# Optimization experiments

Hardware: AMD Instinct MI355X
Metric: run time of the kernel (lower is better)

## Reference

```python
import jax, jax.numpy as jnp
import numpy as np
import itertools

DIM = 384
KEY_DIM = 32
NUM_HEADS = 8
ATTN_RATIO = 4
RESOLUTION = 7
D = ATTN_RATIO * KEY_DIM          # 128
DH = D * NUM_HEADS                # 1024
H_QKV = DH + 2 * KEY_DIM * NUM_HEADS  # 1536
B = 2048
N = RESOLUTION ** 2               # 49


def _build_bias_idxs():
    points = list(itertools.product(range(RESOLUTION), range(RESOLUTION)))
    attention_offsets = {}
    idxs = []
    for p1 in points:
        for p2 in points:
            offset = (abs(p1[0] - p2[0]), abs(p1[1] - p2[1]))
            if offset not in attention_offsets:
                attention_offsets[offset] = len(attention_offsets)
            idxs.append(attention_offsets[offset])
    return np.array(idxs, dtype=np.int32).reshape(N, N), len(attention_offsets)


def setup_inputs() -> dict:
    key = jax.random.key(0)
    ks = jax.random.split(key, 6)
    bias_idxs_np, n_offsets = _build_bias_idxs()  # n_offsets == 49 for resolution 7
    x = jax.random.normal(ks[0], (B, N, DIM), dtype=jnp.float32)
    qkv_w = jax.random.normal(ks[1], (H_QKV, DIM), dtype=jnp.float32) * (DIM ** -0.5)
    qkv_b = jnp.zeros((H_QKV,), dtype=jnp.float32)
    proj_w = jax.random.normal(ks[2], (DIM, DH), dtype=jnp.float32) * (DH ** -0.5)
    proj_b = jnp.zeros((DIM,), dtype=jnp.float32)
    attn_bias = jax.random.normal(ks[3], (NUM_HEADS, n_offsets), dtype=jnp.float32) * 0.02
    bias_idxs = jnp.asarray(bias_idxs_np)
    return {"x": x, "qkv_w": qkv_w, "qkv_b": qkv_b, "proj_w": proj_w,
            "proj_b": proj_b, "attn_bias": attn_bias, "bias_idxs": bias_idxs}


def reference(x, qkv_w, qkv_b, proj_w, proj_b, attn_bias, bias_idxs):
    Bb, Nn, _ = x.shape
    scale = KEY_DIM ** -0.5
    qkv = x @ qkv_w.T + qkv_b                       # [B, N, 1536]
    qkv = qkv.reshape(Bb, Nn, NUM_HEADS, KEY_DIM + KEY_DIM + D)
    q = qkv[..., :KEY_DIM]                          # [B, N, H, kd]
    k = qkv[..., KEY_DIM:2 * KEY_DIM]               # [B, N, H, kd]
    v = qkv[..., 2 * KEY_DIM:]                      # [B, N, H, d]
    bias = attn_bias[:, bias_idxs]                  # [H, N, N] gathered rel-pos bias
    attn = jnp.einsum('bnhk,bmhk->bhnm', q, k) * scale + bias
    attn = jax.nn.softmax(attn, axis=-1)
    out = jnp.einsum('bhnm,bmhd->bnhd', attn, v).reshape(Bb, Nn, DH)
    return out @ proj_w.T + proj_b                  # [B, N, dim]
```

## Files before the change

### kernel.cpp

```cpp
#include <hip/hip_runtime.h>
#include <cstddef>
#include <cstdint>

#define TOK    49
#define KD     32
#define NH     8
#define DHEAD  128
#define HQKV   1536
#define DHTOT  1024
#define DIMM   384

typedef unsigned short u16;
typedef float  f32x4  __attribute__((ext_vector_type(4)));
typedef __bf16 bf16x8 __attribute__((ext_vector_type(8)));

typedef const __attribute__((address_space(1))) void gas_void;
typedef __attribute__((address_space(3))) void las_void;

static __device__ __forceinline__ u16 f2bf(float f) {
    unsigned int u = __builtin_bit_cast(unsigned int, f);
    return (u16)((u + 0x7fffu + ((u >> 16) & 1u)) >> 16);
}

static __device__ __forceinline__ int swz(int row, int c) {
    return (row << 6) + ((((c >> 3) ^ (row & 7)) << 3) | (c & 7));
}

static __device__ __forceinline__ int swzV(int row, int c) {
    return (row << 6) + ((((c >> 3) ^ (row & 7) ^ ((row >> 3) & 7)) << 3) | (c & 7));
}

static __device__ __forceinline__ int xcd_chunk(int bid, int nwg) {
    const int xcd = bid & 7, slot = bid >> 3;
    const int q = nwg >> 3, r = nwg & 7;
    return (xcd < r ? xcd * (q + 1) : r * (q + 1) + (xcd - r) * q) + slot;
}

#define BAR() __builtin_amdgcn_s_barrier()
#define WAIT_VM8() asm volatile("s_waitcnt vmcnt(8)" ::: "memory")
#define WAIT_VM0() asm volatile("s_waitcnt vmcnt(0)" ::: "memory")
#define LGKM0_BAR() do { asm volatile("s_waitcnt lgkmcnt(0)" ::: "memory"); \
                         __builtin_amdgcn_s_barrier(); } while (0)

__global__ __launch_bounds__(256)
void cast_swz(const float* __restrict__ in, u16* __restrict__ out, int K8, long nchunk)
{
    long i = (long)blockIdx.x * 256 + threadIdx.x;
    const long stride = (long)gridDim.x * 256;
    for (; i < nchunk; i += stride) {
        const long row = i / K8;
        const int  c8  = (int)(i - row * K8);
        const int  slot = c8 & 7, tpan = c8 >> 3;
        float4 v0 = reinterpret_cast<const float4*>(in)[i * 2];
        float4 v1 = reinterpret_cast<const float4*>(in)[i * 2 + 1];
        uint4 o;
        o.x = f2bf(v0.x) | ((unsigned)f2bf(v0.y) << 16);
        o.y = f2bf(v0.z) | ((unsigned)f2bf(v0.w) << 16);
        o.z = f2bf(v1.x) | ((unsigned)f2bf(v1.y) << 16);
        o.w = f2bf(v1.z) | ((unsigned)f2bf(v1.w) << 16);
        *reinterpret_cast<uint4*>(out + row * (long)K8 * 8 + tpan * 64 +
                                  ((slot ^ ((int)row & 7)) << 3)) = o;
    }
}

__global__ __launch_bounds__(256)
void bias_expand(const float* __restrict__ attn_bias, const int* __restrict__ idxs,
                 float* __restrict__ bias_full, int n_off)
{
    int i = blockIdx.x * 256 + threadIdx.x;
    if (i < NH * TOK * TOK) {
        int h = i / (TOK * TOK), s = i - h * (TOK * TOK);
        bias_full[i] = attn_bias[h * n_off + idxs[s]];
    }
}

static __device__ __forceinline__ int frag_off(int row, int ks8fg) {
    return (row << 6) + (((ks8fg ^ (row & 7)) << 3));
}

__global__ __launch_bounds__(256)
void gemm_qkv(const u16* __restrict__ A,
              const u16* __restrict__ W,
              const float* __restrict__ bias,
              u16* __restrict__ qkvb, int M)
{
    const int K = DIMM;
    const int NB = HQKV / 128;
    const int nwg = (M / 128) * NB;
    const int wgid = xcd_chunk(blockIdx.x, nwg);
    const int bm = (wgid / NB) * 128;
    const int bn = (wgid % NB) * 128;

    __shared__ u16 Alds[2][128 * 64];
    __shared__ u16 Blds[2][128 * 64];

    const int t    = threadIdx.x;
    const int lane = t & 63;
    const int wv   = t >> 6;
    const int wr   = wv >> 1;
    const int wc   = wv & 1;

    const int lrow = lane >> 3;
    const int lcol = (lane & 7) * 8;
    const int frow = lane & 15;
    const int fg   = lane >> 4;

    f32x4 acc[4][4];
    #pragma unroll
    for (int mi = 0; mi < 4; ++mi)
        #pragma unroll
        for (int ni = 0; ni < 4; ++ni) acc[mi][ni] = (f32x4)0.0f;

    auto STAGE = [&](int buf, int k0) {
        #pragma unroll
        for (int i = 0; i < 4; ++i) {
            const int c   = i * 4 + wv;
            const int row = c * 8 + lrow;
            __builtin_amdgcn_global_load_lds((gas_void*)(A + (size_t)(bm + row) * K + k0 + lcol),
                                             (las_void*)(&Alds[buf][c * 512]), 16, 0, 0);
            __builtin_amdgcn_global_load_lds((gas_void*)(W + (size_t)(bn + row) * K + k0 + lcol),
                                             (las_void*)(&Blds[buf][c * 512]), 16, 0, 0);
        }
    };

    STAGE(0, 0);
    STAGE(1, 64);

    const int NT = 6;
    for (int ts = 0; ts < NT; ++ts) {
        if (ts < NT - 1) { WAIT_VM8(); }
        else             { WAIT_VM0(); }
        BAR();
        const u16* Ab = Alds[ts & 1];
        const u16* Bb = Blds[ts & 1];
        #pragma unroll
        for (int ks = 0; ks < 2; ++ks) {
            const int sl = ks * 4 + fg;
            bf16x8 af[4], bf[4];
            #pragma unroll
            for (int mi = 0; mi < 4; ++mi)
                af[mi] = *reinterpret_cast<const bf16x8*>(&Ab[frag_off(wr * 64 + mi * 16 + frow, sl)]);
            #pragma unroll
            for (int ni = 0; ni < 4; ++ni)
                bf[ni] = *reinterpret_cast<const bf16x8*>(&Bb[frag_off(wc * 64 + ni * 16 + frow, sl)]);
            #pragma unroll
            for (int mi = 0; mi < 4; ++mi)
                #pragma unroll
                for (int ni = 0; ni < 4; ++ni)
                    acc[mi][ni] = __builtin_amdgcn_mfma_f32_16x16x32_bf16(af[mi], bf[ni], acc[mi][ni], 0, 0, 0);
        }
        BAR();
        if (ts < NT - 2) STAGE(ts & 1, (ts + 2) * 64);
    }

    const int rbase = (lane >> 4) * 4;
    #pragma unroll
    for (int ni = 0; ni < 4; ++ni) {
        const int col = bn + wc * 64 + ni * 16 + frow;
        const float bv = bias[col];
        #pragma unroll
        for (int mi = 0; mi < 4; ++mi) {
            #pragma unroll
            for (int j = 0; j < 4; ++j) {
                const int row = bm + wr * 64 + mi * 16 + rbase + j;
                qkvb[(size_t)row * HQKV + col] = f2bf(acc[mi][ni][j] + bv);
            }
        }
    }
}

__global__ __launch_bounds__(256)
void gemm_bf16_nt(const u16* __restrict__ A, const u16* __restrict__ W,
                  const float* __restrict__ bias, float* __restrict__ C,
                  int M, int N, int K)
{
    const int NB = N / 128;
    const int nwg = (M / 128) * NB;
    const int wgid = xcd_chunk(blockIdx.x, nwg);
    const int bm = (wgid / NB) * 128;
    const int bn = (wgid % NB) * 128;

    __shared__ u16 Alds[2][128 * 64];
    __shared__ u16 Blds[2][128 * 64];

    const int t    = threadIdx.x;
    const int lane = t & 63;
    const int wv   = t >> 6;
    const int wr   = wv >> 1;
    const int wc   = wv & 1;

    const int lrow = lane >> 3;
    const int lcol = (lane & 7) * 8;
    const int frow = lane & 15;
    const int fg   = lane >> 4;

    f32x4 acc[4][4];
    #pragma unroll
    for (int mi = 0; mi < 4; ++mi)
        #pragma unroll
        for (int ni = 0; ni < 4; ++ni) acc[mi][ni] = (f32x4)0.0f;

    auto STAGE = [&](int buf, int k0) {
        #pragma unroll
        for (int i = 0; i < 4; ++i) {
            const int c   = i * 4 + wv;
            const int row = c * 8 + lrow;
            __builtin_amdgcn_global_load_lds((gas_void*)(A + (size_t)(bm + row) * K + k0 + lcol),
                                             (las_void*)(&Alds[buf][c * 512]), 16, 0, 0);
            __builtin_amdgcn_global_load_lds((gas_void*)(W + (size_t)(bn + row) * K + k0 + lcol),
                                             (las_void*)(&Blds[buf][c * 512]), 16, 0, 0);
        }
    };

    const int NT = K / 64;
    STAGE(0, 0);
    STAGE(1, 64);

    for (int ts = 0; ts < NT; ++ts) {
        if (ts < NT - 1) { WAIT_VM8(); }
        else             { WAIT_VM0(); }
        BAR();
        const u16* Ab = Alds[ts & 1];
        const u16* Bb = Blds[ts & 1];
        #pragma unroll
        for (int ks = 0; ks < 2; ++ks) {
            const int sl = ks * 4 + fg;
            bf16x8 af[4], bf[4];
            #pragma unroll
            for (int mi = 0; mi < 4; ++mi)
                af[mi] = *reinterpret_cast<const bf16x8*>(&Ab[frag_off(wr * 64 + mi * 16 + frow, sl)]);
            #pragma unroll
            for (int ni = 0; ni < 4; ++ni)
                bf[ni] = *reinterpret_cast<const bf16x8*>(&Bb[frag_off(wc * 64 + ni * 16 + frow, sl)]);
            #pragma unroll
            for (int mi = 0; mi < 4; ++mi)
                #pragma unroll
                for (int ni = 0; ni < 4; ++ni)
                    acc[mi][ni] = __builtin_amdgcn_mfma_f32_16x16x32_bf16(af[mi], bf[ni], acc[mi][ni], 0, 0, 0);
        }
        BAR();
        if (ts < NT - 2) STAGE(ts & 1, (ts + 2) * 64);
    }

    const int rbase = (lane >> 4) * 4;
    #pragma unroll
    for (int ni = 0; ni < 4; ++ni) {
        const int col = bn + wc * 64 + ni * 16 + frow;
        const float bv = bias[col];
        #pragma unroll
        for (int mi = 0; mi < 4; ++mi) {
            #pragma unroll
            for (int j = 0; j < 4; ++j) {
                const int row = bm + wr * 64 + mi * 16 + rbase + j;
                C[(size_t)row * N + col] = acc[mi][ni][j] + bv;
            }
        }
    }
}

#define NCH 5
struct Regs { uint4 v[NCH]; };

static __device__ __forceinline__ void load_regs(Regs& r, const u16* __restrict__ base, int t)
{
    #pragma unroll
    for (int k = 0; k < NCH; ++k) {
        const int idx = t + k * 256;
        if (idx < TOK * 24) {
            const int n = idx / 24, c = idx - n * 24;
            r.v[k] = *reinterpret_cast<const uint4*>(base + (size_t)n * HQKV + c * 8);
        }
    }
}

static __device__ __forceinline__ void write_lds(const Regs& r, u16* __restrict__ QK,
                                                 u16* __restrict__ V, int t)
{
    #pragma unroll
    for (int k = 0; k < NCH; ++k) {
        const int idx = t + k * 256;
        if (idx < TOK * 24) {
            const int n = idx / 24, c24 = idx - n * 24;
            if (c24 < 8) {
                *reinterpret_cast<uint4*>(&QK[(n << 6) + ((c24 ^ (n & 7)) << 3)]) = r.v[k];
            } else {
                const int d0 = (c24 - 8) * 8;
                u16 vals[8];
                *reinterpret_cast<uint4*>(vals) = r.v[k];
                #pragma unroll
                for (int e = 0; e < 8; ++e)
                    V[swzV(d0 + e, n)] = vals[e];
            }
        }
    }
}

static __device__ __forceinline__ void attn_head(
    const u16* __restrict__ QK, const u16* __restrict__ V,
    float* __restrict__ S, u16* __restrict__ Ps,
    const float* __restrict__ bh_bias, u16* __restrict__ ab,
    int b, int h, int t)
{
    const int lane = t & 63;
    const int w    = t >> 6;
    const int fr   = lane & 15;
    const int fg   = lane >> 4;

    bf16x8 qf = *reinterpret_cast<const bf16x8*>(&QK[swz(16 * w + fr, fg * 8)]);
    f32x4 sacc[4];
    #pragma unroll
    for (int nj = 0; nj < 4; ++nj) {
        bf16x8 kf = *reinterpret_cast<const bf16x8*>(&QK[swz(16 * nj + fr, 32 + fg * 8)]);
        sacc[nj] = __builtin_amdgcn_mfma_f32_16x16x32_bf16(qf, kf, (f32x4)0.0f, 0, 0, 0);
    }

    const float scale = 0.17677669529663687f;
    #pragma unroll
    for (int nj = 0; nj < 4; ++nj) {
        #pragma unroll
        for (int j = 0; j < 4; ++j) {
            const int row = 16 * w + fg * 4 + j;
            const int col = 16 * nj + fr;
            const int rn = row < TOK ? row : TOK - 1;
            const int cm = col < TOK ? col : TOK - 1;
            S[row * 80 + col] = sacc[nj][j] * scale + bh_bias[rn * TOK + cm];
        }
    }
    LGKM0_BAR();

    {
        const int n = t >> 2, j = t & 3;
        const float* Sr = &S[n * 80];
        float v[16];
        #pragma unroll
        for (int e = 0; e < 8; ++e) v[e]     = Sr[8 * j + e];
        #pragma unroll
        for (int e = 0; e < 8; ++e) v[8 + e] = Sr[32 + 8 * j + e];

        float mx = -1e30f;
        #pragma unroll
        for (int e = 0; e < 8; ++e) mx = fmaxf(mx, v[e]);
        #pragma unroll
        for (int e = 0; e < 8; ++e)
            if (32 + 8 * j + e < TOK) mx = fmaxf(mx, v[8 + e]);
        mx = fmaxf(mx, __shfl_xor(mx, 1, 4));
        mx = fmaxf(mx, __shfl_xor(mx, 2, 4));

        float sum = 0.f;
        #pragma unroll
        for (int e = 0; e < 8; ++e) { v[e] = __expf(v[e] - mx); sum += v[e]; }
        #pragma unroll
        for (int e = 0; e < 8; ++e) {
            const float ev = (32 + 8 * j + e < TOK) ? __expf(v[8 + e] - mx) : 0.f;
            v[8 + e] = ev; sum += ev;
        }
        sum += __shfl_xor(sum, 1, 4);
        sum += __shfl_xor(sum, 2, 4);
        const float inv = 1.f / sum;

        uint4 o;
        o.x = f2bf(v[0] * inv)  | ((unsigned)f2bf(v[1] * inv)  << 16);
        o.y = f2bf(v[2] * inv)  | ((unsigned)f2bf(v[3] * inv)  << 16);
        o.z = f2bf(v[4] * inv)  | ((unsigned)f2bf(v[5] * inv)  << 16);
        o.w = f2bf(v[6] * inv)  | ((unsigned)f2bf(v[7] * inv)  << 16);
        *reinterpret_cast<uint4*>(&Ps[swz(n, 8 * j)]) = o;
        o.x = f2bf(v[8] * inv)  | ((unsigned)f2bf(v[9] * inv)  << 16);
        o.y = f2bf(v[10] * inv) | ((unsigned)f2bf(v[11] * inv) << 16);
        o.z = f2bf(v[12] * inv) | ((unsigned)f2bf(v[13] * inv) << 16);
        o.w = f2bf(v[14] * inv) | ((unsigned)f2bf(v[15] * inv) << 16);
        *reinterpret_cast<uint4*>(&Ps[swz(n, 32 + 8 * j)]) = o;
    }
    LGKM0_BAR();

    f32x4 oacc[8];
    #pragma unroll
    for (int nj = 0; nj < 8; ++nj) oacc[nj] = (f32x4)0.0f;
    #pragma unroll
    for (int ks = 0; ks < 2; ++ks) {
        bf16x8 pf = *reinterpret_cast<const bf16x8*>(&Ps[swz(16 * w + fr, ks * 32 + fg * 8)]);
        #pragma unroll
        for (int nj = 0; nj < 8; ++nj) {
            bf16x8 vf = *reinterpret_cast<const bf16x8*>(&V[swzV(16 * nj + fr, ks * 32 + fg * 8)]);
            oacc[nj] = __builtin_amdgcn_mfma_f32_16x16x32_bf16(pf, vf, oacc[nj], 0, 0, 0);
        }
    }

    #pragma unroll
    for (int nj = 0; nj < 8; ++nj) {
        const int d = 16 * nj + fr;
        const int c = h * DHEAD + d;
        const int tp = c >> 6, sl = (c >> 3) & 7, cc = c & 7;
        #pragma unroll
        for (int j = 0; j < 4; ++j) {
            const int n = 16 * w + fg * 4 + j;
            if (n < TOK) {
                const int gr = b * TOK + n;
                ab[(size_t)gr * DHTOT + (tp << 6) + (((sl ^ (gr & 7)) << 3) | cc)] = f2bf(oacc[nj][j]);
            }
        }
    }
}

__global__ __launch_bounds__(256)
void attn_mfma(const u16* __restrict__ qkvb,
               const float* __restrict__ bias_full,
               u16* __restrict__ ab)
{
    __shared__ __align__(16) u16  QKs[64 * 64];
    __shared__ __align__(16) u16  Vts[128 * 64];
    __shared__ __align__(16) float S[64 * 80];
    __shared__ __align__(16) u16  Ps[64 * 64];

    const int t  = threadIdx.x;
    const int b  = blockIdx.x;
    const int h0 = blockIdx.y * 2;
    const int h1 = h0 + 1;
    const u16* base = qkvb + (size_t)b * TOK * HQKV;

    if (t < 128 * 2) {
        const int row = t >> 1, sl = 6 + (t & 1);
        *reinterpret_cast<uint4*>(&Vts[(row << 6) +
            (((sl ^ (row & 7) ^ ((row >> 3) & 7)) & 7) << 3)]) = make_uint4(0, 0, 0, 0);
    }
    __syncthreads();

    const u16* qrow = base + h0 * 192;
    for (int flat = t; flat < TOK * 24; flat += 256) {
        const int n = flat / 24, c24 = flat - n * 24;
        uint4 u = *reinterpret_cast<const uint4*>(qrow + (size_t)n * HQKV + c24 * 8);
        if (c24 < 8) {
            *reinterpret_cast<uint4*>(&QKs[(n << 6) + ((c24 ^ (n & 7)) << 3)]) = u;
        } else {
            const int d0 = (c24 - 8) * 8;
            u16 vals[8];
            *reinterpret_cast<uint4*>(vals) = u;
            #pragma unroll
            for (int e = 0; e < 8; ++e)
                Vts[swzV(d0 + e, n)] = vals[e];
        }
    }

    Regs rb;
    load_regs(rb, base + h1 * 192, t);

    LGKM0_BAR();

    attn_head(QKs, Vts, S, Ps, bias_full + h0 * (TOK * TOK), ab, b, h0, t);
    LGKM0_BAR();

    write_lds(rb, QKs, Vts, t);
    LGKM0_BAR();

    attn_head(QKs, Vts, S, Ps, bias_full + h1 * (TOK * TOK), ab, b, h1, t);
}

extern "C" void kernel_launch(void* const* d_in, const int* in_sizes, int n_in,
                              void* d_out, int out_size, void* d_ws, size_t ws_size,
                              hipStream_t stream)
{
    const float* x         = (const float*)d_in[0];
    const float* qkv_w     = (const float*)d_in[1];
    const float* qkv_b     = (const float*)d_in[2];
    const float* proj_w    = (const float*)d_in[3];
    const float* proj_b    = (const float*)d_in[4];
    const float* attn_bias = (const float*)d_in[5];
    const int*   bias_idxs = (const int*)d_in[6];

    const int Mtot  = in_sizes[0] / DIMM;
    const int Btot  = Mtot / TOK;
    const int n_off = in_sizes[5] / NH;

    const size_t nWq = (size_t)HQKV * DIMM;
    const size_t nWp = (size_t)DIMM * DHTOT;
    float* bias_full = (float*)d_ws;
    u16*   wq        = (u16*)((char*)d_ws + 76832);
    u16*   wp        = wq + nWq;
    u16*   dyn       = wp + nWp;
    const size_t fixed_bytes = 76832 + (nWq + nWp) * sizeof(u16);
    const size_t per_batch = (size_t)TOK * (DIMM + HQKV + DHTOT) * 2;

    if (ws_size <= fixed_bytes) return;
    long BcL = (long)((ws_size - fixed_bytes) / per_batch);
    int Bc = (int)((BcL / 128) * 128);
    if (Bc <= 0) return;
    if (Bc > Btot) Bc = Btot;

    cast_swz<<<dim3(288), 256, 0, stream>>>(qkv_w, wq, DIMM / 8, (long)HQKV * (DIMM / 8));
    cast_swz<<<dim3(192), 256, 0, stream>>>(proj_w, wp, DHTOT / 8, (long)DIMM * (DHTOT / 8));
    bias_expand<<<dim3((NH * TOK * TOK + 255) / 256), 256, 0, stream>>>(attn_bias, bias_idxs, bias_full, n_off);

    for (int b0 = 0; b0 < Btot; b0 += Bc) {
        const int bc = (b0 + Bc <= Btot) ? Bc : (Btot - b0);
        const int Mc = bc * TOK;

        u16* xb   = dyn;
        u16* qkvb = xb   + (size_t)Bc * TOK * DIMM;
        u16* abb  = qkvb + (size_t)Bc * TOK * HQKV;

        const float* xc   = x + (size_t)b0 * TOK * DIMM;
        float*       outc = (float*)d_out + (size_t)b0 * TOK * DIMM;

        cast_swz<<<dim3(2048), 256, 0, stream>>>(xc, xb, DIMM / 8, (long)Mc * (DIMM / 8));

        gemm_qkv<<<dim3((Mc / 128) * (HQKV / 128)), 256, 0, stream>>>(xb, wq, qkv_b, qkvb, Mc);

        attn_mfma<<<dim3(bc, NH / 2), 256, 0, stream>>>(qkvb, bias_full, abb);

        gemm_bf16_nt<<<dim3((Mc / 128) * (DIMM / 128)), 256, 0, stream>>>(abb, wp, proj_b, outc, Mc, DIMM, DHTOT);
    }
}
```

Before: 664.3 us.

## Halve GEMM M-tile to 64 and process four heads per attention block

Both GEMM kernels move from a 128x128 tile with 2x2 waves to a 64x128 tile where each wave covers 64 rows by 32 columns. The A staging and the vmcnt wait drop to match, and the grid doubles. The attention kernel now handles four heads per block instead of two, prefetching the next head's Q/K/V into registers while computing the current one. This trades GEMM operand reuse for more workgroups and better occupancy and tail balance, and it halves the attention grid so per-block setup is amortized over more heads.

```diff
diff --git a/kernel.cpp b/kernel.cpp
--- a/kernel.cpp
+++ b/kernel.cpp
@@ -37,7 +37,7 @@
 }
 
 #define BAR() __builtin_amdgcn_s_barrier()
-#define WAIT_VM8() asm volatile("s_waitcnt vmcnt(8)" ::: "memory")
+#define WAIT_VM6() asm volatile("s_waitcnt vmcnt(6)" ::: "memory")
 #define WAIT_VM0() asm volatile("s_waitcnt vmcnt(0)" ::: "memory")
 #define LGKM0_BAR() do { asm volatile("s_waitcnt lgkmcnt(0)" ::: "memory"); \
                          __builtin_amdgcn_s_barrier(); } while (0)
@@ -86,38 +86,40 @@
 {
     const int K = DIMM;
     const int NB = HQKV / 128;
-    const int nwg = (M / 128) * NB;
+    const int nwg = (M / 64) * NB;
     const int wgid = xcd_chunk(blockIdx.x, nwg);
-    const int bm = (wgid / NB) * 128;
+    const int bm = (wgid / NB) * 64;
     const int bn = (wgid % NB) * 128;
 
-    __shared__ u16 Alds[2][128 * 64];
+    __shared__ u16 Alds[2][64 * 64];
     __shared__ u16 Blds[2][128 * 64];
 
     const int t    = threadIdx.x;
     const int lane = t & 63;
     const int wv   = t >> 6;
-    const int wr   = wv >> 1;
-    const int wc   = wv & 1;
-
     const int lrow = lane >> 3;
     const int lcol = (lane & 7) * 8;
     const int frow = lane & 15;
     const int fg   = lane >> 4;
 
-    f32x4 acc[4][4];
+    f32x4 acc[4][2];
     #pragma unroll
     for (int mi = 0; mi < 4; ++mi)
         #pragma unroll
-        for (int ni = 0; ni < 4; ++ni) acc[mi][ni] = (f32x4)0.0f;
+        for (int nc = 0; nc < 2; ++nc) acc[mi][nc] = (f32x4)0.0f;
 
     auto STAGE = [&](int buf, int k0) {
         #pragma unroll
-        for (int i = 0; i < 4; ++i) {
+        for (int i = 0; i < 2; ++i) {
             const int c   = i * 4 + wv;
             const int row = c * 8 + lrow;
             __builtin_amdgcn_global_load_lds((gas_void*)(A + (size_t)(bm + row) * K + k0 + lcol),
                                              (las_void*)(&Alds[buf][c * 512]), 16, 0, 0);
+        }
+        #pragma unroll
+        for (int i = 0; i < 4; ++i) {
+            const int c   = i * 4 + wv;
+            const int row = c * 8 + lrow;
             __builtin_amdgcn_global_load_lds((gas_void*)(W + (size_t)(bn + row) * K + k0 + lcol),
                                              (las_void*)(&Blds[buf][c * 512]), 16, 0, 0);
         }
@@ -128,7 +130,7 @@
 
     const int NT = 6;
     for (int ts = 0; ts < NT; ++ts) {
-        if (ts < NT - 1) { WAIT_VM8(); }
+        if (ts < NT - 1) { WAIT_VM6(); }
         else             { WAIT_VM0(); }
         BAR();
         const u16* Ab = Alds[ts & 1];
@@ -136,18 +138,18 @@
         #pragma unroll
         for (int ks = 0; ks < 2; ++ks) {
             const int sl = ks * 4 + fg;
-            bf16x8 af[4], bf[4];
+            bf16x8 af[4], bf[2];
             #pragma unroll
             for (int mi = 0; mi < 4; ++mi)
-                af[mi] = *reinterpret_cast<const bf16x8*>(&Ab[frag_off(wr * 64 + mi * 16 + frow, sl)]);
-            #pragma unroll
-            for (int ni = 0; ni < 4; ++ni)
-                bf[ni] = *reinterpret_cast<const bf16x8*>(&Bb[frag_off(wc * 64 + ni * 16 + frow, sl)]);
+                af[mi] = *reinterpret_cast<const bf16x8*>(&Ab[frag_off(mi * 16 + frow, sl)]);
+            #pragma unroll
+            for (int nc = 0; nc < 2; ++nc)
+                bf[nc] = *reinterpret_cast<const bf16x8*>(&Bb[frag_off(wv * 32 + nc * 16 + frow, sl)]);
             #pragma unroll
             for (int mi = 0; mi < 4; ++mi)
                 #pragma unroll
-                for (int ni = 0; ni < 4; ++ni)
-                    acc[mi][ni] = __builtin_amdgcn_mfma_f32_16x16x32_bf16(af[mi], bf[ni], acc[mi][ni], 0, 0, 0);
+                for (int nc = 0; nc < 2; ++nc)
+                    acc[mi][nc] = __builtin_amdgcn_mfma_f32_16x16x32_bf16(af[mi], bf[nc], acc[mi][nc], 0, 0, 0);
         }
         BAR();
         if (ts < NT - 2) STAGE(ts & 1, (ts + 2) * 64);
@@ -155,15 +157,15 @@
 
     const int rbase = (lane >> 4) * 4;
     #pragma unroll
-    for (int ni = 0; ni < 4; ++ni) {
-        const int col = bn + wc * 64 + ni * 16 + frow;
+    for (int nc = 0; nc < 2; ++nc) {
+        const int col = bn + wv * 32 + nc * 16 + frow;
         const float bv = bias[col];
         #pragma unroll
         for (int mi = 0; mi < 4; ++mi) {
             #pragma unroll
             for (int j = 0; j < 4; ++j) {
-                const int row = bm + wr * 64 + mi * 16 + rbase + j;
-                qkvb[(size_t)row * HQKV + col] = f2bf(acc[mi][ni][j] + bv);
+                const int row = bm + mi * 16 + rbase + j;
+                qkvb[(size_t)row * HQKV + col] = f2bf(acc[mi][nc][j] + bv);
             }
         }
     }
@@ -175,38 +177,40 @@
                   int M, int N, int K)
 {
     const int NB = N / 128;
-    const int nwg = (M / 128) * NB;
+    const int nwg = (M / 64) * NB;
     const int wgid = xcd_chunk(blockIdx.x, nwg);
-    const int bm = (wgid / NB) * 128;
+    const int bm = (wgid / NB) * 64;
     const int bn = (wgid % NB) * 128;
 
-    __shared__ u16 Alds[2][128 * 64];
+    __shared__ u16 Alds[2][64 * 64];
     __shared__ u16 Blds[2][128 * 64];
 
     const int t    = threadIdx.x;
     const int lane = t & 63;
     const int wv   = t >> 6;
-    const int wr   = wv >> 1;
-    const int wc   = wv & 1;
-
     const int lrow = lane >> 3;
     const int lcol = (lane & 7) * 8;
     const int frow = lane & 15;
     const int fg   = lane >> 4;
 
-    f32x4 acc[4][4];
+    f32x4 acc[4][2];
     #pragma unroll
     for (int mi = 0; mi < 4; ++mi)
         #pragma unroll
-        for (int ni = 0; ni < 4; ++ni) acc[mi][ni] = (f32x4)0.0f;
+        for (int nc = 0; nc < 2; ++nc) acc[mi][nc] = (f32x4)0.0f;
 
     auto STAGE = [&](int buf, int k0) {
         #pragma unroll
-        for (int i = 0; i < 4; ++i) {
+        for (int i = 0; i < 2; ++i) {
             const int c   = i * 4 + wv;
             const int row = c * 8 + lrow;
             __builtin_amdgcn_global_load_lds((gas_void*)(A + (size_t)(bm + row) * K + k0 + lcol),
                                              (las_void*)(&Alds[buf][c * 512]), 16, 0, 0);
+        }
+        #pragma unroll
+        for (int i = 0; i < 4; ++i) {
+            const int c   = i * 4 + wv;
+            const int row = c * 8 + lrow;
             __builtin_amdgcn_global_load_lds((gas_void*)(W + (size_t)(bn + row) * K + k0 + lcol),
                                              (las_void*)(&Blds[buf][c * 512]), 16, 0, 0);
         }
@@ -217,7 +221,7 @@
     STAGE(1, 64);
 
     for (int ts = 0; ts < NT; ++ts) {
-        if (ts < NT - 1) { WAIT_VM8(); }
+        if (ts < NT - 1) { WAIT_VM6(); }
         else             { WAIT_VM0(); }
         BAR();
         const u16* Ab = Alds[ts & 1];
@@ -225,18 +229,18 @@
         #pragma unroll
         for (int ks = 0; ks < 2; ++ks) {
             const int sl = ks * 4 + fg;
-            bf16x8 af[4], bf[4];
+            bf16x8 af[4], bf[2];
             #pragma unroll
             for (int mi = 0; mi < 4; ++mi)
-                af[mi] = *reinterpret_cast<const bf16x8*>(&Ab[frag_off(wr * 64 + mi * 16 + frow, sl)]);
-            #pragma unroll
-            for (int ni = 0; ni < 4; ++ni)
-                bf[ni] = *reinterpret_cast<const bf16x8*>(&Bb[frag_off(wc * 64 + ni * 16 + frow, sl)]);
+                af[mi] = *reinterpret_cast<const bf16x8*>(&Ab[frag_off(mi * 16 + frow, sl)]);
+            #pragma unroll
+            for (int nc = 0; nc < 2; ++nc)
+                bf[nc] = *reinterpret_cast<const bf16x8*>(&Bb[frag_off(wv * 32 + nc * 16 + frow, sl)]);
             #pragma unroll
             for (int mi = 0; mi < 4; ++mi)
                 #pragma unroll
-                for (int ni = 0; ni < 4; ++ni)
-                    acc[mi][ni] = __builtin_amdgcn_mfma_f32_16x16x32_bf16(af[mi], bf[ni], acc[mi][ni], 0, 0, 0);
+                for (int nc = 0; nc < 2; ++nc)
+                    acc[mi][nc] = __builtin_amdgcn_mfma_f32_16x16x32_bf16(af[mi], bf[nc], acc[mi][nc], 0, 0, 0);
         }
         BAR();
         if (ts < NT - 2) STAGE(ts & 1, (ts + 2) * 64);
@@ -244,15 +248,15 @@
 
     const int rbase = (lane >> 4) * 4;
     #pragma unroll
-    for (int ni = 0; ni < 4; ++ni) {
-        const int col = bn + wc * 64 + ni * 16 + frow;
+    for (int nc = 0; nc < 2; ++nc) {
+        const int col = bn + wv * 32 + nc * 16 + frow;
         const float bv = bias[col];
         #pragma unroll
         for (int mi = 0; mi < 4; ++mi) {
             #pragma unroll
             for (int j = 0; j < 4; ++j) {
-                const int row = bm + wr * 64 + mi * 16 + rbase + j;
-                C[(size_t)row * N + col] = acc[mi][ni][j] + bv;
+                const int row = bm + mi * 16 + rbase + j;
+                C[(size_t)row * N + col] = acc[mi][nc][j] + bv;
             }
         }
     }
@@ -413,8 +417,7 @@
 
     const int t  = threadIdx.x;
     const int b  = blockIdx.x;
-    const int h0 = blockIdx.y * 2;
-    const int h1 = h0 + 1;
+    const int h0 = blockIdx.y * 4;
     const u16* base = qkvb + (size_t)b * TOK * HQKV;
 
     if (t < 128 * 2) {
@@ -440,18 +443,15 @@
         }
     }
 
-    Regs rb;
-    load_regs(rb, base + h1 * 192, t);
-
-    LGKM0_BAR();
-
-    attn_head(QKs, Vts, S, Ps, bias_full + h0 * (TOK * TOK), ab, b, h0, t);
-    LGKM0_BAR();
-
-    write_lds(rb, QKs, Vts, t);
-    LGKM0_BAR();
-
-    attn_head(QKs, Vts, S, Ps, bias_full + h1 * (TOK * TOK), ab, b, h1, t);
+    Regs r;
+    #pragma unroll
+    for (int i = 0; i < 4; ++i) {
+        if (i > 0) write_lds(r, QKs, Vts, t);
+        if (i < 3) load_regs(r, base + (h0 + i + 1) * 192, t);
+        LGKM0_BAR();
+        attn_head(QKs, Vts, S, Ps, bias_full + (h0 + i) * (TOK * TOK), ab, b, h0 + i, t);
+        LGKM0_BAR();
+    }
 }
 
 extern "C" void kernel_launch(void* const* d_in, const int* in_sizes, int n_in,
@@ -502,10 +502,10 @@
 
         cast_swz<<<dim3(2048), 256, 0, stream>>>(xc, xb, DIMM / 8, (long)Mc * (DIMM / 8));
 
-        gemm_qkv<<<dim3((Mc / 128) * (HQKV / 128)), 256, 0, stream>>>(xb, wq, qkv_b, qkvb, Mc);
-
-        attn_mfma<<<dim3(bc, NH / 2), 256, 0, stream>>>(qkvb, bias_full, abb);
-
-        gemm_bf16_nt<<<dim3((Mc / 128) * (DIMM / 128)), 256, 0, stream>>>(abb, wp, proj_b, outc, Mc, DIMM, DHTOT);
-    }
-}
+        gemm_qkv<<<dim3((Mc / 64) * (HQKV / 128)), 256, 0, stream>>>(xb, wq, qkv_b, qkvb, Mc);
+
+        attn_mfma<<<dim3(bc, NH / 4), 256, 0, stream>>>(qkvb, bias_full, abb);
+
+        gemm_bf16_nt<<<dim3((Mc / 64) * (DIMM / 128)), 256, 0, stream>>>(abb, wp, proj_b, outc, Mc, DIMM, DHTOT);
+    }
+}
```

Result: no change. 652.7 us (-1.7%).
